# Performance work log

Measured on AMD Instinct MI355X. Metric: run time of the kernel, lower is better.

## Reference

```python
import jax, jax.numpy as jnp
import numpy as np
from jax import lax

DN = ('NCHW', 'OIHW', 'NCHW')


def conv3x3(x, w, b):
    y = lax.conv_general_dilated(x, w, (1, 1), [(1, 1), (1, 1)], dimension_numbers=DN)
    return y + b[None, :, None, None]


def lrelu(x, s):
    return jnp.where(x >= 0, x, s * x)


def layernorm_c(x, g, b, eps=1e-5):
    # LayerNorm over embed_dim; tokens are (h,w), so normalize the channel axis
    m = jnp.mean(x, axis=1, keepdims=True)
    v = jnp.var(x, axis=1, keepdims=True)
    return (x - m) / jnp.sqrt(v + eps) * g[None, :, None, None] + b[None, :, None, None]


def bilateral_corr(x1, x2, md):
    # bilateral cost volume on L2-normalized features:
    # out[b,d,h,w] = <x1n[b,:,h-dy,w-dx], x2n[b,:,h+dy,w+dx]>, (dy,dx) in [-md,md]^2
    def l2n(x):
        return x / jnp.maximum(jnp.linalg.norm(x, axis=1, keepdims=True), 1e-12)
    x1n, x2n = l2n(x1), l2n(x2)
    B, C, H, W = x1.shape
    p1 = jnp.pad(x1n, ((0, 0), (0, 0), (md, md), (md, md)))
    p2 = jnp.pad(x2n, ((0, 0), (0, 0), (md, md), (md, md)))
    outs = []
    for dy in range(-md, md + 1):
        for dx in range(-md, md + 1):
            a = p1[:, :, md - dy:md - dy + H, md - dx:md - dx + W]
            b = p2[:, :, md + dy:md + dy + H, md + dx:md + dx + W]
            outs.append(jnp.sum(a * b, axis=1))
    return jnp.stack(outs, axis=1)  # [B, (2md+1)^2, H, W]


def tail(xt, bi, gln, bln, w0, b0, wr1, br1, wr2, br2, w2, b2, w3, b3, wdec, bdec, wf, bf):
    xt = layernorm_c(xt, gln, bln)
    y = conv3x3(jnp.concatenate([xt, bi], axis=1), w0, b0)
    # resblock(64,64): lrelu(conv2(lrelu(conv1(y))) + y), slope 0.1
    s = y
    r = lrelu(conv3x3(y, wr1, br1), 0.1)
    r = conv3x3(r, wr2, br2) + s
    y = lrelu(r, 0.1)
    y = lrelu(conv3x3(y, w2, b2), 0.2)
    y = lrelu(conv3x3(y, w3, b3), 0.2)
    # ConvTranspose2d(64,64,3,stride=2,pad=1,out_pad=1): lhs-dilated conv with flipped kernel
    wd = jnp.transpose(jnp.flip(wdec, (-2, -1)), (1, 0, 2, 3))  # torch [in,out,kh,kw] -> OIHW
    y = lax.conv_general_dilated(y, wd, (1, 1), [(1, 2), (1, 2)], lhs_dilation=(2, 2), dimension_numbers=DN) + bdec[None, :, None, None]
    flow = conv3x3(y, wf, bf)  # [B, 2, 2H, 2W]
    B, _, H2, W2 = flow.shape
    # F.interpolate(scale_factor=4, mode='bilinear', align_corners=False) * 4
    return jax.image.resize(flow, (B, 2, 4 * H2, 4 * W2), method='bilinear') * 4.0


def setup_inputs():
    key = jax.random.key(0)
    ks = jax.random.split(key, 16)
    B, C, H, W = 4, 256, 96, 160
    md = 3
    r = lambda k, s, sc=0.05: jax.random.normal(k, s, jnp.float32) * sc
    return {
        'x1': jax.random.normal(ks[0], (B, C, H, W), jnp.float32),
        'x2': jax.random.normal(ks[1], (B, C, H, W), jnp.float32),
        'xt': jax.random.normal(ks[2], (B, C, H, W), jnp.float32),
        'gln': jnp.ones((C,), jnp.float32),
        'bln': jnp.zeros((C,), jnp.float32),
        'w0': r(ks[3], (64, C + (2 * md + 1) ** 2, 3, 3)),
        'b0': jnp.zeros((64,), jnp.float32),
        'wr1': r(ks[4], (64, 64, 3, 3)), 'br1': jnp.zeros((64,), jnp.float32),
        'wr2': r(ks[5], (64, 64, 3, 3)), 'br2': jnp.zeros((64,), jnp.float32),
        'w2': r(ks[6], (64, 64, 3, 3)), 'b2': jnp.zeros((64,), jnp.float32),
        'w3': r(ks[7], (64, 64, 3, 3)), 'b3': jnp.zeros((64,), jnp.float32),
        'wdec': r(ks[8], (64, 64, 3, 3)), 'bdec': jnp.zeros((64,), jnp.float32),
        'wf': r(ks[9], (2, 64, 3, 3)), 'bf': jnp.zeros((2,), jnp.float32),
        'corr_range': 3,
    }


def reference(x1, x2, xt, gln, bln, w0, b0, wr1, br1, wr2, br2, w2, b2, w3, b3, wdec, bdec, wf, bf, corr_range):
    bi = bilateral_corr(x1, x2, int(corr_range))
    return tail(xt, bi, gln, bln, w0, b0, wr1, br1, wr2, br2, w2, b2, w3, b3, wdec, bdec, wf, bf)
```

## Files before the change

kernel.cpp:

```cpp
#include <hip/hip_runtime.h>
#include <math.h>

#define HH_ 96
#define WW_ 160
#define HW 15360
#define NPIX 61440
#define CC 256
#define C0 320
#define FF 64
#define H2 192
#define W2 320
#define OHW 61440
#define HO 768
#define WO 1280

typedef __attribute__((ext_vector_type(8))) short short8;
typedef __attribute__((ext_vector_type(4))) float f32x4;

__device__ __forceinline__ float bf2f(ushort u) {
    union { unsigned int i; float f; } v; v.i = ((unsigned int)u) << 16; return v.f;
}
__device__ __forceinline__ ushort f2bf(float f) {
    union { float f; unsigned int i; } v; v.f = f;
    unsigned int u = v.i;
    return (ushort)((u + 0x7FFFu + ((u >> 16) & 1u)) >> 16);
}

__global__ __launch_bounds__(256) void normpack_kernel(
    const float* __restrict__ x1, const float* __restrict__ x2, const float* __restrict__ xt,
    const float* __restrict__ gam, const float* __restrict__ bet,
    ushort* __restrict__ x1c, ushort* __restrict__ x2c,
    ushort* __restrict__ Xhi) {
    __shared__ float tile[32 * 265];
    const int t = threadIdx.x;
    const int pxt = blockIdx.x, which = blockIdx.y, b = blockIdx.z;
    const float* src = (which == 0 ? x1 : which == 1 ? x2 : xt);
    src += (size_t)b * CC * HW + pxt * 32;

    {
        int px_l = t & 31, c_hi = t >> 5;
#pragma unroll 8
        for (int i = 0; i < 32; ++i) {
            int c = i * 8 + c_hi;
            tile[px_l * 265 + c + (c >> 5)] = src[(size_t)c * HW + px_l];
        }
    }
    __syncthreads();

    const int px = t >> 3, oct = t & 7;
    float s1 = 0.f, s2 = 0.f;
    {
        const float* row = &tile[px * 265 + oct * 33];
#pragma unroll
        for (int i = 0; i < 32; ++i) {
            float v = row[(i + oct * 4) & 31];
            s1 += v; s2 += v * v;
        }
    }
    s1 += __shfl_xor(s1, 1); s1 += __shfl_xor(s1, 2); s1 += __shfl_xor(s1, 4);
    s2 += __shfl_xor(s2, 1); s2 += __shfl_xor(s2, 2); s2 += __shfl_xor(s2, 4);

    const int p = b * HW + pxt * 32 + px;
    const float* row = &tile[px * 265 + oct * 33];
    if (which < 2) {
        float inv = 1.f / fmaxf(sqrtf(s2), 1e-12f);
        ushort* dst = (which == 0 ? x1c : x2c);
        size_t ob = (size_t)p * CC + oct * 32;
#pragma unroll
        for (int g = 0; g < 4; ++g) {
            short8 v;
#pragma unroll
            for (int j = 0; j < 8; ++j)
                v[j] = (short)f2bf(row[g * 8 + j] * inv);
            *(short8*)(dst + ob + g * 8) = v;
        }
    } else {
        float m = s1 * (1.f / 256.f);
        float var = fmaxf(s2 * (1.f / 256.f) - m * m, 0.f);
        float rs = rsqrtf(var + 1e-5f);
        size_t ob = (size_t)p * C0 + oct * 32;
#pragma unroll
        for (int g = 0; g < 4; ++g) {
            short8 vh;
#pragma unroll
            for (int j = 0; j < 8; ++j) {
                int c = oct * 32 + g * 8 + j;
                vh[j] = (short)f2bf((row[g * 8 + j] - m) * rs * gam[c] + bet[c]);
            }
            *(short8*)(Xhi + ob + g * 8) = vh;
        }
        short8 z = {0, 0, 0, 0, 0, 0, 0, 0};
        *(short8*)(Xhi + (size_t)p * C0 + 256 + oct * 8) = z;
    }
}

__global__ __launch_bounds__(256) void corr_mfma_kernel(
    const ushort* __restrict__ x1c, const ushort* __restrict__ x2c,
    ushort* __restrict__ Xhi) {
    const int lane = threadIdx.x & 63;
    const int wv = threadIdx.x >> 6;
    const int sid = ((blockIdx.x & 7) * 120) + (blockIdx.x >> 3);
    const int b  = sid / 240;
    const int rem = sid % 240;
    const int uq = rem / 10, xt = rem % 10;
    const int u = uq * 4 + wv;
    const int x0 = xt * 16;
    const int jl = lane & 15;
    const int kg = lane >> 4;
    const short8 zero8 = {0, 0, 0, 0, 0, 0, 0, 0};

    short8 qf[8];
    {
        size_t qb = ((size_t)b * HW + u * WW_ + x0 + jl) * CC + kg * 8;
#pragma unroll
        for (int ks = 0; ks < 8; ++ks)
            qf[ks] = *(const short8*)(x1c + qb + ks * 32);
    }

    for (int dy = -3; dy <= 3; ++dy) {
        const int y = u + dy;
        if ((unsigned)y >= (unsigned)HH_) continue;
        const int w = u + 2 * dy;
        const bool rowok = (unsigned)w < (unsigned)HH_;

        f32x4 acc0 = (f32x4){0.f, 0.f, 0.f, 0.f};
        f32x4 acc1 = (f32x4){0.f, 0.f, 0.f, 0.f};
        if (rowok) {
#pragma unroll
            for (int nt = 0; nt < 2; ++nt) {
                int kx = x0 - 6 + jl + 16 * nt;
                bool ok = (unsigned)kx < (unsigned)WW_;
                int kxc = min(max(kx, 0), WW_ - 1);
                size_t kb = ((size_t)b * HW + w * WW_ + kxc) * CC + kg * 8;
#pragma unroll
                for (int ks = 0; ks < 8; ++ks) {
                    short8 bv = *(const short8*)(x2c + kb + ks * 32);
                    if (!ok) bv = zero8;
                    if (nt == 0)
                        acc0 = __builtin_amdgcn_mfma_f32_16x16x32_bf16(qf[ks], bv, acc0, 0, 0, 0);
                    else
                        acc1 = __builtin_amdgcn_mfma_f32_16x16x32_bf16(qf[ks], bv, acc1, 0, 0, 0);
                }
            }
        }
#pragma unroll
        for (int nt = 0; nt < 2; ++nt) {
            int j = jl + 16 * nt;
#pragma unroll
            for (int r = 0; r < 4; ++r) {
                int q = kg * 4 + r;
                int tt = j - q - 6;
                if (tt & 1) continue;
                int dx = tt >> 1;
                if (dx < -3 || dx > 3) continue;
                int cx = x0 + q + dx;
                if ((unsigned)cx >= (unsigned)WW_) continue;
                float v = rowok ? (nt == 0 ? acc0[r] : acc1[r]) : 0.f;
                size_t o = ((size_t)(b * HW + y * WW_ + cx)) * C0
                         + 256 + (dy + 3) * 7 + (dx + 3);
                Xhi[o] = f2bf(v);
            }
        }
    }
}

__global__ void pack_w_all(const float* __restrict__ w0, const float* __restrict__ wr1,
                           const float* __restrict__ wr2, const float* __restrict__ w2,
                           const float* __restrict__ w3, const float* __restrict__ wdec,
                           ushort* __restrict__ W0, ushort* __restrict__ WR1,
                           ushort* __restrict__ WR2, ushort* __restrict__ W2o,
                           ushort* __restrict__ W3o, ushort* __restrict__ WD) {
    int job = blockIdx.y;
    const float* w = job == 0 ? w0 : job == 1 ? wr1 : job == 2 ? wr2
                   : job == 3 ? w2 : job == 4 ? w3 : wdec;
    ushort* dst = job == 0 ? W0 : job == 1 ? WR1 : job == 2 ? WR2
                : job == 3 ? W2o : job == 4 ? W3o : WD;
    int CinReal = job == 0 ? 305 : 64;
    int KC = job == 0 ? 10 : 2;
    int isDeconv = (job == 5);
    int gid = blockIdx.x * blockDim.x + threadIdx.x;
    int total = 9 * KC * 4 * 64;
    if (gid >= total) return;
    int lane = gid & 63;
    int nt = (gid >> 6) & 3;
    int kc = (gid >> 8) % KC;
    int slot = (gid >> 8) / KC;
    int co = nt * 16 + (lane & 15);
    int ky = slot / 3, kx = slot % 3;
    for (int j = 0; j < 8; ++j) {
        int ci = kc * 32 + (lane >> 4) * 8 + j;
        float v = 0.f;
        if (ci < CinReal) {
            if (isDeconv) v = w[((size_t)(ci * 64 + co) * 3 + (2 - ky)) * 3 + (2 - kx)];
            else          v = w[((size_t)(co * CinReal + ci) * 3 + ky) * 3 + kx];
        }
        dst[(size_t)gid * 8 + j] = f2bf(v);
    }
}

template<int KC>
__global__ __launch_bounds__(256, 4) void conv_lds_t(
    const ushort* __restrict__ Ahi,
    const ushort* __restrict__ Whi,
    const float* __restrict__ bias,
    ushort* __restrict__ Ohi,
    const ushort* __restrict__ Rhi,
    float slope, int act, int hasres) {
    constexpr int CIN = KC * 32;
    __shared__ ushort lds[2 * 3488];
    const int t = threadIdx.x;
    const int lane = t & 63;
    const int wave = t >> 6;
    const int kg = lane >> 4;
    const int jl = lane & 15;
    const short8 zero8 = {0, 0, 0, 0, 0, 0, 0, 0};

    const int sid = ((blockIdx.x & 7) * 120) + (blockIdx.x >> 3);
    const int b0 = sid / 240;
    const int rm = sid % 240;
    const int yq = rm / 10, xw = rm % 10;
    const int y0 = yq * 4;
    const int x0 = xw * 16;
    const size_t rowbase = (size_t)b0 * HW;

    f32x4 acc[4];
#pragma unroll
    for (int nt = 0; nt < 4; ++nt) acc[nt] = (f32x4){0.f, 0.f, 0.f, 0.f};

    auto stage = [&](ushort* buf, int kc) {
#pragma unroll
        for (int i = 0; i < 2; ++i) {
            int e = t + i * 256;
            if (e < 432) {
                int kge = e & 3;
                int q = e >> 2;
                int pe = q % 18;
                int re = q / 18;
                int gy = y0 - 1 + re, gx = x0 - 1 + pe;
                bool ok = ((unsigned)gy < 96u) && ((unsigned)gx < 160u);
                short8 vh = zero8;
                if (ok) {
                    size_t ga = ((rowbase + gy * WW_ + gx) * (size_t)CIN) + kc * 32 + kge * 8;
                    vh = *(const short8*)(Ahi + ga);
                }
                *(short8*)(buf + kge * 872 + (re * 18 + pe) * 8) = vh;
            }
        }
    };

    stage(lds, 0);

#pragma unroll 1
    for (int kc = 0; kc < KC; ++kc) {
        __syncthreads();
        if (kc + 1 < KC) stage(lds + ((kc + 1) & 1) * 3488, kc + 1);
        const ushort* bufc = lds + (kc & 1) * 3488;
#pragma unroll
        for (int tap = 0; tap < 9; ++tap) {
            const int dy = tap / 3 - 1, dx = tap % 3 - 1;
            const int abase = kg * 872 + (wave + dy + 1) * 144 + (jl + dx + 1) * 8;
            short8 ah = *(const short8*)(bufc + abase);
            const ushort* wt = Whi + (size_t)(tap * KC + kc) * 2048;
#pragma unroll
            for (int nt = 0; nt < 4; ++nt) {
                short8 bh = *(const short8*)(wt + (nt * 64 + lane) * 8);
                acc[nt] = __builtin_amdgcn_mfma_f32_16x16x32_bf16(ah, bh, acc[nt], 0, 0, 0);
            }
        }
    }

#pragma unroll
    for (int r = 0; r < 4; ++r) {
        size_t pr = rowbase + (y0 + wave) * WW_ + x0 + kg * 4 + r;
#pragma unroll
        for (int nt = 0; nt < 4; ++nt) {
            int co = nt * 16 + jl;
            float vv = acc[nt][r] + bias[co];
            size_t oo = pr * 64 + co;
            if (hasres) vv += bf2f(Rhi[oo]);
            if (act) vv = vv >= 0.f ? vv : vv * slope;
            Ohi[oo] = f2bf(vv);
        }
    }
}

__global__ __launch_bounds__(256, 2) void deconv_fused_kernel(
    const ushort* __restrict__ Ahi,
    const ushort* __restrict__ Whi,
    const float* __restrict__ bias,
    float* __restrict__ dec) {
    const int lane = threadIdx.x & 63;
    const int wave = threadIdx.x >> 6;
    const int kg = lane >> 4;
    const short8 zero8 = {0, 0, 0, 0, 0, 0, 0, 0};

    const int sid = ((blockIdx.x & 7) * 120) + (blockIdx.x >> 3);
    const int b0 = sid / 240;
    const int rm = sid % 240;
    const int yq = rm / 10, xh = rm % 10;
    const int y0 = yq * 4 + wave;
    const int x0 = xh * 16;
    const size_t rowbase = (size_t)b0 * HW;

    f32x4 acc[4][4];
#pragma unroll
    for (int p = 0; p < 4; ++p)
#pragma unroll
        for (int nt = 0; nt < 4; ++nt) acc[p][nt] = (f32x4){0.f, 0.f, 0.f, 0.f};

    const int nuse[4]   = {4, 2, 2, 1};
    const int upar[4][4] = {{0, 1, 2, 3}, {1, 3, -1, -1}, {2, 3, -1, -1}, {3, -1, -1, -1}};
    const int uslt[4][4] = {{4, 3, 1, 0}, {5, 2, -1, -1}, {7, 6, -1, -1}, {8, -1, -1, -1}};

#pragma unroll
    for (int o = 0; o < 4; ++o) {
        const int ody = o >> 1, odx = o & 1;
        int yy = y0 + ody, xx = x0 + (lane & 15) + odx;
        bool v = (unsigned)yy < 96u && (unsigned)xx < 160u;
        int yyc = min(yy, 95), xxc = min(xx, 159);
        size_t a = (rowbase + yyc * WW_ + xxc) * 64 + kg * 8;
#pragma unroll
        for (int kc = 0; kc < 2; ++kc) {
            short8 ah = *(const short8*)(Ahi + a + kc * 32);
            if (!v) ah = zero8;
#pragma unroll
            for (int u = 0; u < 4; ++u) {
                if (u >= nuse[o]) break;
                int par = upar[o][u], slot = uslt[o][u];
#pragma unroll
                for (int nt = 0; nt < 4; ++nt) {
                    short8 bh = *(const short8*)(Whi + ((size_t)slot * 2 + kc) * 2048
                                                 + ((size_t)nt * 64 + lane) * 8);
                    acc[par][nt] = __builtin_amdgcn_mfma_f32_16x16x32_bf16(ah, bh, acc[par][nt], 0, 0, 0);
                }
            }
        }
    }

#pragma unroll
    for (int r = 0; r < 4; ++r) {
        int x2 = x0 + kg * 4 + r;
#pragma unroll
        for (int par = 0; par < 4; ++par) {
            int py = par >> 1, px = par & 1;
            size_t po = ((size_t)b0 * H2 + 2 * y0 + py) * W2 + 2 * x2 + px;
#pragma unroll
            for (int nt = 0; nt < 4; ++nt) {
                int co = nt * 16 + (lane & 15);
                dec[po * 64 + co] = acc[par][nt][r] + bias[co];
            }
        }
    }
}

__global__ __launch_bounds__(256) void flow_kernel(const float* __restrict__ dec,
                                                   const float* __restrict__ wf,
                                                   const float* __restrict__ bf2v,
                                                   float* __restrict__ flow) {
    __shared__ float wsm[1152];
    for (int i = threadIdx.x; i < 1152; i += 256) wsm[i] = wf[i];
    __syncthreads();
    int fid = ((blockIdx.x & 7) * 120) + (blockIdx.x >> 3);
    int p = fid * 256 + threadIdx.x;
    if (p >= 4 * OHW) return;
    int b = p / OHW, rem = p % OHW, oy = rem / W2, ox = rem % W2;
    float a0 = bf2v[0], a1 = bf2v[1];
    for (int ky = 0; ky < 3; ++ky) {
        int yy = oy + ky - 1;
        if ((unsigned)yy >= (unsigned)H2) continue;
        for (int kx = 0; kx < 3; ++kx) {
            int xx = ox + kx - 1;
            if ((unsigned)xx >= (unsigned)W2) continue;
            size_t base = ((size_t)b * OHW + yy * W2 + xx) * 64;
            int tap = ky * 3 + kx;
#pragma unroll
            for (int c4 = 0; c4 < 16; ++c4) {
                f32x4 v = *(const f32x4*)(dec + base + c4 * 4);
#pragma unroll
                for (int j = 0; j < 4; ++j) {
                    int ci = c4 * 4 + j;
                    a0 += v[j] * wsm[ci * 9 + tap];
                    a1 += v[j] * wsm[(64 + ci) * 9 + tap];
                }
            }
        }
    }
    flow[(size_t)(b * 2 + 0) * OHW + rem] = a0;
    flow[(size_t)(b * 2 + 1) * OHW + rem] = a1;
}

__global__ void resize_kernel(const float* __restrict__ flow, float* __restrict__ out) {
    int idx = blockIdx.x * blockDim.x + threadIdx.x;
    int total = 4 * 2 * HO * WO;
    if (idx >= total) return;
    int ox = idx % WO;
    int oy = (idx / WO) % HO;
    int c = (idx / (WO * HO)) % 2;
    int b = idx / (WO * HO * 2);
    float sy = (oy + 0.5f) * 0.25f - 0.5f;
    float sx = (ox + 0.5f) * 0.25f - 0.5f;
    int y0 = (int)floorf(sy);
    int x0 = (int)floorf(sx);
    float fy = sy - y0;
    float fx = sx - x0;
    int y0c = min(max(y0, 0), H2 - 1);
    int y1c = min(max(y0 + 1, 0), H2 - 1);
    int x0c = min(max(x0, 0), W2 - 1);
    int x1c = min(max(x0 + 1, 0), W2 - 1);
    const float* fb = flow + (size_t)(b * 2 + c) * OHW;
    float v00 = fb[y0c * W2 + x0c];
    float v01 = fb[y0c * W2 + x1c];
    float v10 = fb[y1c * W2 + x0c];
    float v11 = fb[y1c * W2 + x1c];
    float v = (1.f - fy) * ((1.f - fx) * v00 + fx * v01)
            + fy * ((1.f - fx) * v10 + fx * v11);
    out[idx] = v * 4.0f;
}

extern "C" void kernel_launch(void* const* d_in, const int* in_sizes, int n_in,
                              void* d_out, int out_size, void* d_ws, size_t ws_size,
                              hipStream_t stream) {
    const float* x1   = (const float*)d_in[0];
    const float* x2   = (const float*)d_in[1];
    const float* xt   = (const float*)d_in[2];
    const float* gln  = (const float*)d_in[3];
    const float* bln  = (const float*)d_in[4];
    const float* w0   = (const float*)d_in[5];
    const float* b0   = (const float*)d_in[6];
    const float* wr1  = (const float*)d_in[7];
    const float* br1  = (const float*)d_in[8];
    const float* wr2  = (const float*)d_in[9];
    const float* br2  = (const float*)d_in[10];
    const float* w2   = (const float*)d_in[11];
    const float* b2   = (const float*)d_in[12];
    const float* w3   = (const float*)d_in[13];
    const float* b3   = (const float*)d_in[14];
    const float* wdec = (const float*)d_in[15];
    const float* bdec = (const float*)d_in[16];
    const float* wf   = (const float*)d_in[17];
    const float* bfv  = (const float*)d_in[18];
    float* out = (float*)d_out;

    char* ws = (char*)d_ws;
    ushort* x1c  = (ushort*)(ws + 0);
    ushort* x2c  = (ushort*)(ws + 31457280);
    ushort* X0hi = (ushort*)(ws + 62914560);
    ushort* y0hi = (ushort*)(ws + 102236160);
    ushort* t1hi = (ushort*)(ws + 110100480);
    ushort* t2hi = (ushort*)(ws + 117964800);
    float*  dec  = (float*)(ws + 0);
    float*  flowb = (float*)(ws + 62914560);
    char* wp = ws + 125829120;
    ushort* W0hi  = (ushort*)(wp);
    ushort* WR1hi = (ushort*)(wp + 368640);
    ushort* WR2hi = (ushort*)(wp + 442368);
    ushort* W2hi  = (ushort*)(wp + 516096);
    ushort* W3hi  = (ushort*)(wp + 589824);
    ushort* WDhi  = (ushort*)(wp + 663552);

    pack_w_all<<<dim3(90, 6), 256, 0, stream>>>(w0, wr1, wr2, w2, w3, wdec,
        W0hi, WR1hi, WR2hi, W2hi, W3hi, WDhi);

    normpack_kernel<<<dim3(480, 3, 4), 256, 0, stream>>>(
        x1, x2, xt, gln, bln, x1c, x2c, X0hi);
    corr_mfma_kernel<<<960, 256, 0, stream>>>(x1c, x2c, X0hi);

    conv_lds_t<10><<<960, 256, 0, stream>>>(X0hi, W0hi, b0, y0hi, nullptr, 0.f, 0, 0);
    conv_lds_t<2><<<960, 256, 0, stream>>>(y0hi, WR1hi, br1, t1hi, nullptr, 0.1f, 1, 0);
    conv_lds_t<2><<<960, 256, 0, stream>>>(t1hi, WR2hi, br2, t2hi, y0hi, 0.1f, 1, 1);
    conv_lds_t<2><<<960, 256, 0, stream>>>(t2hi, W2hi, b2, t1hi, nullptr, 0.2f, 1, 0);
    conv_lds_t<2><<<960, 256, 0, stream>>>(t1hi, W3hi, b3, t2hi, nullptr, 0.2f, 1, 0);
    deconv_fused_kernel<<<960, 256, 0, stream>>>(t2hi, WDhi, bdec, dec);

    flow_kernel<<<960, 256, 0, stream>>>(dec, wf, bfv, flowb);
    resize_kernel<<<30720, 256, 0, stream>>>(flowb, out);

    (void)in_sizes; (void)n_in; (void)out_size; (void)ws_size;
}
```

Baseline: 369.1 us.

## Store deconv output as bf16 and retile normpack to 16-pixel blocks

The deconvolution output feeding the flow conv is now written as bf16 instead of fp32, which halves the intermediate's write and read traffic (about 63 MB down to 31 MB). The flow kernel reads it with 16-byte short8 loads. Separately, the normalisation/pack kernel now handles 16 pixels per block with 16 threads per pixel, doubling the grid and halving LDS use, with a wider shuffle reduction. The bf16 intermediate adds rounding error to the final flow output.

```diff
diff --git a/kernel.cpp b/kernel.cpp
--- a/kernel.cpp
+++ b/kernel.cpp
@@ -31,66 +31,62 @@
     const float* __restrict__ gam, const float* __restrict__ bet,
     ushort* __restrict__ x1c, ushort* __restrict__ x2c,
     ushort* __restrict__ Xhi) {
-    __shared__ float tile[32 * 265];
+    __shared__ float tile[16 * 265];
     const int t = threadIdx.x;
     const int pxt = blockIdx.x, which = blockIdx.y, b = blockIdx.z;
     const float* src = (which == 0 ? x1 : which == 1 ? x2 : xt);
-    src += (size_t)b * CC * HW + pxt * 32;
+    src += (size_t)b * CC * HW + pxt * 16;
 
     {
-        int px_l = t & 31, c_hi = t >> 5;
-#pragma unroll 8
-        for (int i = 0; i < 32; ++i) {
-            int c = i * 8 + c_hi;
+        int px_l = t & 15, c_hi = t >> 4;
+#pragma unroll
+        for (int i = 0; i < 16; ++i) {
+            int c = i * 16 + c_hi;
             tile[px_l * 265 + c + (c >> 5)] = src[(size_t)c * HW + px_l];
         }
     }
     __syncthreads();
 
-    const int px = t >> 3, oct = t & 7;
+    const int px = t >> 4, grp = t & 15;
+    const float* row = &tile[px * 265 + grp * 16 + (grp >> 1)];
+    float v[16];
     float s1 = 0.f, s2 = 0.f;
-    {
-        const float* row = &tile[px * 265 + oct * 33];
-#pragma unroll
-        for (int i = 0; i < 32; ++i) {
-            float v = row[(i + oct * 4) & 31];
-            s1 += v; s2 += v * v;
-        }
-    }
-    s1 += __shfl_xor(s1, 1); s1 += __shfl_xor(s1, 2); s1 += __shfl_xor(s1, 4);
-    s2 += __shfl_xor(s2, 1); s2 += __shfl_xor(s2, 2); s2 += __shfl_xor(s2, 4);
-
-    const int p = b * HW + pxt * 32 + px;
-    const float* row = &tile[px * 265 + oct * 33];
+#pragma unroll
+    for (int j = 0; j < 16; ++j) { float f = row[j]; v[j] = f; s1 += f; s2 += f * f; }
+    s1 += __shfl_xor(s1, 1); s1 += __shfl_xor(s1, 2); s1 += __shfl_xor(s1, 4); s1 += __shfl_xor(s1, 8);
+    s2 += __shfl_xor(s2, 1); s2 += __shfl_xor(s2, 2); s2 += __shfl_xor(s2, 4); s2 += __shfl_xor(s2, 8);
+
+    const int p = b * HW + pxt * 16 + px;
     if (which < 2) {
         float inv = 1.f / fmaxf(sqrtf(s2), 1e-12f);
         ushort* dst = (which == 0 ? x1c : x2c);
-        size_t ob = (size_t)p * CC + oct * 32;
-#pragma unroll
-        for (int g = 0; g < 4; ++g) {
-            short8 v;
-#pragma unroll
-            for (int j = 0; j < 8; ++j)
-                v[j] = (short)f2bf(row[g * 8 + j] * inv);
-            *(short8*)(dst + ob + g * 8) = v;
-        }
+        size_t ob = (size_t)p * CC + grp * 16;
+        short8 o0, o1;
+#pragma unroll
+        for (int j = 0; j < 8; ++j) {
+            o0[j] = (short)f2bf(v[j] * inv);
+            o1[j] = (short)f2bf(v[8 + j] * inv);
+        }
+        *(short8*)(dst + ob) = o0;
+        *(short8*)(dst + ob + 8) = o1;
     } else {
         float m = s1 * (1.f / 256.f);
         float var = fmaxf(s2 * (1.f / 256.f) - m * m, 0.f);
         float rs = rsqrtf(var + 1e-5f);
-        size_t ob = (size_t)p * C0 + oct * 32;
-#pragma unroll
-        for (int g = 0; g < 4; ++g) {
-            short8 vh;
-#pragma unroll
-            for (int j = 0; j < 8; ++j) {
-                int c = oct * 32 + g * 8 + j;
-                vh[j] = (short)f2bf((row[g * 8 + j] - m) * rs * gam[c] + bet[c]);
-            }
-            *(short8*)(Xhi + ob + g * 8) = vh;
-        }
-        short8 z = {0, 0, 0, 0, 0, 0, 0, 0};
-        *(short8*)(Xhi + (size_t)p * C0 + 256 + oct * 8) = z;
+        size_t ob = (size_t)p * C0 + grp * 16;
+        short8 o0, o1;
+#pragma unroll
+        for (int j = 0; j < 8; ++j) {
+            int c = grp * 16 + j;
+            o0[j] = (short)f2bf((v[j] - m) * rs * gam[c] + bet[c]);
+            o1[j] = (short)f2bf((v[8 + j] - m) * rs * gam[c + 8] + bet[c + 8]);
+        }
+        *(short8*)(Xhi + ob) = o0;
+        *(short8*)(Xhi + ob + 8) = o1;
+        if (grp < 8) {
+            short8 z = {0, 0, 0, 0, 0, 0, 0, 0};
+            *(short8*)(Xhi + (size_t)p * C0 + 256 + grp * 8) = z;
+        }
     }
 }
 
@@ -288,7 +284,7 @@
     const ushort* __restrict__ Ahi,
     const ushort* __restrict__ Whi,
     const float* __restrict__ bias,
-    float* __restrict__ dec) {
+    ushort* __restrict__ decb) {
     const int lane = threadIdx.x & 63;
     const int wave = threadIdx.x >> 6;
     const int kg = lane >> 4;
@@ -347,13 +343,13 @@
 #pragma unroll
             for (int nt = 0; nt < 4; ++nt) {
                 int co = nt * 16 + (lane & 15);
-                dec[po * 64 + co] = acc[par][nt][r] + bias[co];
-            }
-        }
-    }
-}
-
-__global__ __launch_bounds__(256) void flow_kernel(const float* __restrict__ dec,
+                decb[po * 64 + co] = f2bf(acc[par][nt][r] + bias[co]);
+            }
+        }
+    }
+}
+
+__global__ __launch_bounds__(256) void flow_kernel(const ushort* __restrict__ decb,
                                                    const float* __restrict__ wf,
                                                    const float* __restrict__ bf2v,
                                                    float* __restrict__ flow) {
@@ -374,13 +370,14 @@
             size_t base = ((size_t)b * OHW + yy * W2 + xx) * 64;
             int tap = ky * 3 + kx;
 #pragma unroll
-            for (int c4 = 0; c4 < 16; ++c4) {
-                f32x4 v = *(const f32x4*)(dec + base + c4 * 4);
-#pragma unroll
-                for (int j = 0; j < 4; ++j) {
-                    int ci = c4 * 4 + j;
-                    a0 += v[j] * wsm[ci * 9 + tap];
-                    a1 += v[j] * wsm[(64 + ci) * 9 + tap];
+            for (int c8 = 0; c8 < 8; ++c8) {
+                short8 v8 = *(const short8*)(decb + base + c8 * 8);
+#pragma unroll
+                for (int j = 0; j < 8; ++j) {
+                    float f = bf2f((ushort)v8[j]);
+                    int ci = c8 * 8 + j;
+                    a0 += f * wsm[ci * 9 + tap];
+                    a1 += f * wsm[(64 + ci) * 9 + tap];
                 }
             }
         }
@@ -448,7 +445,7 @@
     ushort* y0hi = (ushort*)(ws + 102236160);
     ushort* t1hi = (ushort*)(ws + 110100480);
     ushort* t2hi = (ushort*)(ws + 117964800);
-    float*  dec  = (float*)(ws + 0);
+    ushort* decb = (ushort*)(ws + 0);
     float*  flowb = (float*)(ws + 62914560);
     char* wp = ws + 125829120;
     ushort* W0hi  = (ushort*)(wp);
@@ -461,7 +458,7 @@
     pack_w_all<<<dim3(90, 6), 256, 0, stream>>>(w0, wr1, wr2, w2, w3, wdec,
         W0hi, WR1hi, WR2hi, W2hi, W3hi, WDhi);
 
-    normpack_kernel<<<dim3(480, 3, 4), 256, 0, stream>>>(
+    normpack_kernel<<<dim3(960, 3, 4), 256, 0, stream>>>(
         x1, x2, xt, gln, bln, x1c, x2c, X0hi);
     corr_mfma_kernel<<<960, 256, 0, stream>>>(x1c, x2c, X0hi);
 
@@ -470,9 +467,9 @@
     conv_lds_t<2><<<960, 256, 0, stream>>>(t1hi, WR2hi, br2, t2hi, y0hi, 0.1f, 1, 1);
     conv_lds_t<2><<<960, 256, 0, stream>>>(t2hi, W2hi, b2, t1hi, nullptr, 0.2f, 1, 0);
     conv_lds_t<2><<<960, 256, 0, stream>>>(t1hi, W3hi, b3, t2hi, nullptr, 0.2f, 1, 0);
-    deconv_fused_kernel<<<960, 256, 0, stream>>>(t2hi, WDhi, bdec, dec);
-
-    flow_kernel<<<960, 256, 0, stream>>>(dec, wf, bfv, flowb);
+    deconv_fused_kernel<<<960, 256, 0, stream>>>(t2hi, WDhi, bdec, decb);
+
+    flow_kernel<<<960, 256, 0, stream>>>(decb, wf, bfv, flowb);
     resize_kernel<<<30720, 256, 0, stream>>>(flowb, out);
 
     (void)in_sizes; (void)n_in; (void)out_size; (void)ws_size;
```

New measurement: 380.4 us. +3.1%, slower.
